# Optimization experiments

Hardware: AMD Instinct MI355X
Metric: run time of the kernel (lower is better)

The kernel has to match this reference:

```python
import jax, jax.numpy as jnp
import numpy as np

EPS = 1e-5

def _face_normals(v, vi):
    # v: [B,V,3], vi: [F,3] -> [B,F,3]
    pts = v[:, vi]                                  # [B,F,3,3]
    n = jnp.cross(pts[:, :, 1] - pts[:, :, 0], pts[:, :, 2] - pts[:, :, 0])
    norm = jnp.linalg.norm(n, axis=-1, keepdims=True)
    return n / jnp.where(norm < EPS, 1.0, norm)

def _vert_normals(v, vi):
    fn = _face_normals(v, vi)                       # [B,F,3]
    fn_rep = jnp.repeat(fn, 3, axis=1)              # [B,3F,3] (one copy per face vertex)
    vn = jnp.zeros_like(v).at[:, vi.reshape(-1)].add(fn_rep)
    norm = jnp.linalg.norm(vn, axis=-1, keepdims=True)
    return vn / jnp.where(norm < EPS, 1.0, norm)

def _values_to_uv(values, index_image, bary_image):
    # values: [B,V,C]; index_image/bary_image: [U,U,3] -> [B,C,U,U]
    mask = jnp.all(index_image != -1, axis=-1)      # [U,U]
    idx = jnp.clip(index_image, 0, values.shape[1] - 1)
    vals = values[:, idx]                           # [B,U,U,3,C]
    uv = jnp.einsum('buvkc,uvk->bcuv', vals, bary_image.astype(values.dtype))
    return uv * mask[None, None].astype(values.dtype)

def _grid_sample_bilinear(img, gx, gy):
    # img: [B,C,H,W]; gx,gy: [N] in [-1,1]; align_corners=False, zero padding
    B, C, H, W = img.shape
    ix = ((gx + 1.0) * W - 1.0) * 0.5
    iy = ((gy + 1.0) * H - 1.0) * 0.5
    x0 = jnp.floor(ix); y0 = jnp.floor(iy)
    x1 = x0 + 1.0;      y1 = y0 + 1.0
    wx1 = ix - x0; wx0 = 1.0 - wx1
    wy1 = iy - y0; wy0 = 1.0 - wy1
    def gather(xi, yi):
        valid = (xi >= 0) & (xi < W) & (yi >= 0) & (yi < H)
        xc = jnp.clip(xi, 0, W - 1).astype(jnp.int32)
        yc = jnp.clip(yi, 0, H - 1).astype(jnp.int32)
        return img[:, :, yc, xc] * valid.astype(img.dtype)  # [B,C,N]
    return (gather(x0, y0) * (wx0 * wy0) + gather(x1, y0) * (wx1 * wy0)
          + gather(x0, y1) * (wx0 * wy1) + gather(x1, y1) * (wx1 * wy1))

def _sample_uv(values_uv, uv_coords, v2uv):
    g = uv_coords * 2.0 - 1.0                       # [T,2]
    vals = _grid_sample_bilinear(values_uv, g[:, 0], g[:, 1])  # [B,C,T]
    vals = jnp.transpose(vals, (0, 2, 1))           # [B,T,C]
    return vals[:, v2uv].mean(axis=2)               # [B,V,C]

def setup_inputs() -> dict:
    key = jax.random.key(0)
    ks = jax.random.split(key, 6)
    B, V, Fc, U, T, K = 8, 100000, 200000, 1024, 110000, 2
    verts = jax.random.normal(ks[0], (B, V, 3), jnp.float32)
    vi = jax.random.randint(ks[1], (Fc, 3), 0, V, dtype=jnp.int32)
    index_image = jax.random.randint(ks[2], (U, U, 3), 0, V, dtype=jnp.int32)
    bary_image = jax.random.uniform(ks[3], (U, U, 3), jnp.float32)
    vt = jax.random.uniform(ks[4], (T, 2), jnp.float32)
    v2uv = jax.random.randint(ks[5], (V, K), 0, T, dtype=jnp.int32)
    return {"verts": verts, "bary_image": bary_image, "vt": vt,
            "vi": vi, "index_image": index_image, "v2uv": v2uv}

def reference(verts, bary_image, vt, vi, index_image, v2uv):
    vn = _vert_normals(verts, vi)                   # [B,V,3]
    uv = _values_to_uv(vn, index_image, bary_image) # [B,3,U,U]
    return _sample_uv(uv, vt, v2uv)                 # [B,V,3]
```

## Files before the change

kernel.cpp:

```cpp
#include <hip/hip_runtime.h>

#define EPS 1e-5f

constexpr int B = 8;
constexpr int V = 100000;
constexpr int F = 200000;
constexpr int U = 1024;
constexpr int T = 110000;
constexpr int ELLCAP = 32;
constexpr int TRB = (V + 255) / 256;
constexpr int ELB = (3 * F + 255) / 256;

__global__ void pre_kernel(const float* __restrict__ verts,
                           float4* __restrict__ vertsT,
                           const int* __restrict__ vi,
                           int* __restrict__ cnt,
                           int* __restrict__ ell) {
    int blk = blockIdx.x;
    if (blk < TRB) {
        int v = blk * 256 + threadIdx.x;
        if (v >= V) return;
        float4 row[8];
#pragma unroll
        for (int b = 0; b < 8; ++b) {
            const float* p = verts + (size_t)b * V * 3 + (size_t)v * 3;
            row[b] = make_float4(p[0], p[1], p[2], 0.0f);
        }
        float4* dst = vertsT + (size_t)v * 8;
#pragma unroll
        for (int b = 0; b < 8; ++b) dst[b] = row[b];
    } else {
        int e = (blk - TRB) * 256 + threadIdx.x;
        if (e >= 3 * F) return;
        int v = vi[e];
        int pos = atomicAdd(&cnt[v], 1);
        if (pos < ELLCAP) ell[v * ELLCAP + pos] = e / 3;
    }
}

__global__ void face_normals(const float4* __restrict__ vertsT,
                             const int* __restrict__ vi,
                             float4* __restrict__ fn) {
    int id = blockIdx.x * blockDim.x + threadIdx.x;
    if (id >= F * 8) return;
    int f = id >> 3;
    int b = id & 7;

    int i0 = vi[f * 3 + 0];
    int i1 = vi[f * 3 + 1];
    int i2 = vi[f * 3 + 2];

    float4 p0 = vertsT[(size_t)i0 * 8 + b];
    float4 p1 = vertsT[(size_t)i1 * 8 + b];
    float4 p2 = vertsT[(size_t)i2 * 8 + b];

    float e1x = p1.x - p0.x, e1y = p1.y - p0.y, e1z = p1.z - p0.z;
    float e2x = p2.x - p0.x, e2y = p2.y - p0.y, e2z = p2.z - p0.z;

    float nx = e1y * e2z - e1z * e2y;
    float ny = e1z * e2x - e1x * e2z;
    float nz = e1x * e2y - e1y * e2x;

    float norm = sqrtf(nx * nx + ny * ny + nz * nz);
    float inv = (norm < EPS) ? 1.0f : (1.0f / norm);
    fn[id] = make_float4(nx * inv, ny * inv, nz * inv, 0.0f);
}

__global__ void gather_vn(const float4* __restrict__ fn,
                          const int* __restrict__ cnt,
                          const int* __restrict__ ell,
                          float4* __restrict__ vn) {
    int id = blockIdx.x * blockDim.x + threadIdx.x;
    if (id >= V * 8) return;
    int v = id >> 3;
    int b = id & 7;

    int deg = min(cnt[v], ELLCAP);
    const int* row = ell + (size_t)v * ELLCAP;

    float ax = 0.0f, ay = 0.0f, az = 0.0f;
    for (int j = 0; j < deg; ++j) {
        int f = row[j];
        float4 n = fn[(size_t)f * 8 + b];
        ax += n.x; ay += n.y; az += n.z;
    }

    float n = sqrtf(ax * ax + ay * ay + az * az);
    float inv = (n < EPS) ? 1.0f : (1.0f / n);
    vn[id] = make_float4(ax * inv, ay * inv, az * inv, 0.0f);
}

__global__ void sample_points(const float4* __restrict__ vn,
                              const int* __restrict__ index_image,
                              const float* __restrict__ bary_image,
                              const float* __restrict__ vt,
                              float4* __restrict__ vals) {
    int id = blockIdx.x * blockDim.x + threadIdx.x;
    if (id >= T * 8) return;
    int t = id >> 3;
    int b = id & 7;

    float gx = vt[t * 2 + 0];
    float gy = vt[t * 2 + 1];
    float ix = gx * (float)U - 0.5f;
    float iy = gy * (float)U - 0.5f;

    float x0f = floorf(ix);
    float y0f = floorf(iy);
    int x0 = (int)x0f;
    int y0 = (int)y0f;
    float wx1 = ix - x0f, wx0 = 1.0f - wx1;
    float wy1 = iy - y0f, wy0 = 1.0f - wy1;

    float ax = 0.0f, ay = 0.0f, az = 0.0f;

#pragma unroll
    for (int cy = 0; cy < 2; ++cy) {
        int y = y0 + cy;
        if (y < 0 || y >= U) continue;
        float wy = cy ? wy1 : wy0;
#pragma unroll
        for (int cx = 0; cx < 2; ++cx) {
            int x = x0 + cx;
            if (x < 0 || x >= U) continue;
            float w = wy * (cx ? wx1 : wx0);

            int pix = y * U + x;
            int i0 = index_image[pix * 3 + 0];
            int i1 = index_image[pix * 3 + 1];
            int i2 = index_image[pix * 3 + 2];
            float m = (i0 != -1 && i1 != -1 && i2 != -1) ? 1.0f : 0.0f;
            i0 = min(max(i0, 0), V - 1);
            i1 = min(max(i1, 0), V - 1);
            i2 = min(max(i2, 0), V - 1);

            float b0 = bary_image[pix * 3 + 0];
            float b1 = bary_image[pix * 3 + 1];
            float b2 = bary_image[pix * 3 + 2];

            float4 q0 = vn[(size_t)i0 * 8 + b];
            float4 q1 = vn[(size_t)i1 * 8 + b];
            float4 q2 = vn[(size_t)i2 * 8 + b];

            float wm = w * m;
            float wb0 = wm * b0, wb1 = wm * b1, wb2 = wm * b2;
            ax += wb0 * q0.x + wb1 * q1.x + wb2 * q2.x;
            ay += wb0 * q0.y + wb1 * q1.y + wb2 * q2.y;
            az += wb0 * q0.z + wb1 * q1.z + wb2 * q2.z;
        }
    }

    vals[id] = make_float4(ax, ay, az, 0.0f);
}

__global__ void gather_out(const float4* __restrict__ vals,
                           const int* __restrict__ v2uv,
                           float* __restrict__ out) {
    int id = blockIdx.x * blockDim.x + threadIdx.x;
    if (id >= V * 8) return;
    int v = id >> 3;
    int b = id & 7;

    int t0 = v2uv[v * 2 + 0];
    int t1 = v2uv[v * 2 + 1];
    float4 x = vals[(size_t)t0 * 8 + b];
    float4 y = vals[(size_t)t1 * 8 + b];

    float* o = out + (size_t)b * V * 3 + (size_t)v * 3;
    o[0] = 0.5f * (x.x + y.x);
    o[1] = 0.5f * (x.y + y.y);
    o[2] = 0.5f * (x.z + y.z);
}

extern "C" void kernel_launch(void* const* d_in, const int* in_sizes, int n_in,
                              void* d_out, int out_size, void* d_ws, size_t ws_size,
                              hipStream_t stream) {
    const float* verts   = (const float*)d_in[0];
    const float* bary    = (const float*)d_in[1];
    const float* vt      = (const float*)d_in[2];
    const int*   vi      = (const int*)d_in[3];
    const int*   idx_img = (const int*)d_in[4];
    const int*   v2uv    = (const int*)d_in[5];
    float* out = (float*)d_out;

    float4* vertsT = (float4*)d_ws;
    float4* vn     = vertsT;
    float4* fn     = vertsT + (size_t)V * 8;
    float4* vals   = fn;
    int*    cnt    = (int*)(fn + (size_t)F * 8);
    int*    ell    = cnt + V;

    hipMemsetAsync(cnt, 0, (size_t)V * sizeof(int), stream);

    const int BLK = 256;
    pre_kernel<<<TRB + ELB, BLK, 0, stream>>>(verts, vertsT, vi, cnt, ell);
    face_normals<<<(F * 8 + BLK - 1) / BLK, BLK, 0, stream>>>(vertsT, vi, fn);
    gather_vn<<<(V * 8 + BLK - 1) / BLK, BLK, 0, stream>>>(fn, cnt, ell, vn);
    sample_points<<<(T * 8 + BLK - 1) / BLK, BLK, 0, stream>>>(
        vn, idx_img, bary, vt, vals);
    gather_out<<<(V * 8 + BLK - 1) / BLK, BLK, 0, stream>>>(vals, v2uv, out);
}
```

Before: 207.8 us.

## Fuse ELL build, face normals and per-texel corner precompute into one launch

The memset is replaced by zeroing the counters inside the transpose kernel. ELL construction, face-normal computation and a new per-texel corner precompute (index-image lookup, mask, bilinear and barycentric weights) are merged into one kernel. sample_points then reads the compact Corner records instead of recomputing them for each of the 8 batches. This cuts launches and removes redundant index/bary image loads, at the cost of an extra workspace buffer and writing and reading the corner array.

Measured after the change: 208.0 us. About the same (+0.1%).

```diff
diff --git a/kernel.cpp b/kernel.cpp
--- a/kernel.cpp
+++ b/kernel.cpp
@@ -8,14 +8,18 @@
 constexpr int U = 1024;
 constexpr int T = 110000;
 constexpr int ELLCAP = 32;
+
 constexpr int TRB = (V + 255) / 256;
+constexpr int CZB = (V + 255) / 256;
 constexpr int ELB = (3 * F + 255) / 256;
-
-__global__ void pre_kernel(const float* __restrict__ verts,
-                           float4* __restrict__ vertsT,
-                           const int* __restrict__ vi,
-                           int* __restrict__ cnt,
-                           int* __restrict__ ell) {
+constexpr int FNB = (F * 8 + 255) / 256;
+constexpr int CPB = (T + 255) / 256;
+
+struct Corner { int i0, i1, i2; float w0, w1, w2; };
+
+__global__ void k1_pre(const float* __restrict__ verts,
+                       float4* __restrict__ vertsT,
+                       int* __restrict__ cnt) {
     int blk = blockIdx.x;
     if (blk < TRB) {
         int v = blk * 256 + threadIdx.x;
@@ -30,40 +34,99 @@
 #pragma unroll
         for (int b = 0; b < 8; ++b) dst[b] = row[b];
     } else {
-        int e = (blk - TRB) * 256 + threadIdx.x;
+        int i = (blk - TRB) * 256 + threadIdx.x;
+        if (i < V) cnt[i] = 0;
+    }
+}
+
+__global__ void k2_fused(const int* __restrict__ vi,
+                         int* __restrict__ cnt,
+                         int* __restrict__ ell,
+                         const float4* __restrict__ vertsT,
+                         float4* __restrict__ fn,
+                         const int* __restrict__ index_image,
+                         const float* __restrict__ bary_image,
+                         const float* __restrict__ vt,
+                         Corner* __restrict__ corners) {
+    int blk = blockIdx.x;
+
+    if (blk < ELB) {
+        int e = blk * 256 + threadIdx.x;
         if (e >= 3 * F) return;
         int v = vi[e];
         int pos = atomicAdd(&cnt[v], 1);
         if (pos < ELLCAP) ell[v * ELLCAP + pos] = e / 3;
-    }
-}
-
-__global__ void face_normals(const float4* __restrict__ vertsT,
-                             const int* __restrict__ vi,
-                             float4* __restrict__ fn) {
-    int id = blockIdx.x * blockDim.x + threadIdx.x;
-    if (id >= F * 8) return;
-    int f = id >> 3;
-    int b = id & 7;
-
-    int i0 = vi[f * 3 + 0];
-    int i1 = vi[f * 3 + 1];
-    int i2 = vi[f * 3 + 2];
-
-    float4 p0 = vertsT[(size_t)i0 * 8 + b];
-    float4 p1 = vertsT[(size_t)i1 * 8 + b];
-    float4 p2 = vertsT[(size_t)i2 * 8 + b];
-
-    float e1x = p1.x - p0.x, e1y = p1.y - p0.y, e1z = p1.z - p0.z;
-    float e2x = p2.x - p0.x, e2y = p2.y - p0.y, e2z = p2.z - p0.z;
-
-    float nx = e1y * e2z - e1z * e2y;
-    float ny = e1z * e2x - e1x * e2z;
-    float nz = e1x * e2y - e1y * e2x;
-
-    float norm = sqrtf(nx * nx + ny * ny + nz * nz);
-    float inv = (norm < EPS) ? 1.0f : (1.0f / norm);
-    fn[id] = make_float4(nx * inv, ny * inv, nz * inv, 0.0f);
+        return;
+    }
+
+    if (blk < ELB + FNB) {
+        int id = (blk - ELB) * 256 + threadIdx.x;
+        if (id >= F * 8) return;
+        int f = id >> 3;
+        int b = id & 7;
+
+        int i0 = vi[f * 3 + 0];
+        int i1 = vi[f * 3 + 1];
+        int i2 = vi[f * 3 + 2];
+
+        float4 p0 = vertsT[(size_t)i0 * 8 + b];
+        float4 p1 = vertsT[(size_t)i1 * 8 + b];
+        float4 p2 = vertsT[(size_t)i2 * 8 + b];
+
+        float e1x = p1.x - p0.x, e1y = p1.y - p0.y, e1z = p1.z - p0.z;
+        float e2x = p2.x - p0.x, e2y = p2.y - p0.y, e2z = p2.z - p0.z;
+
+        float nx = e1y * e2z - e1z * e2y;
+        float ny = e1z * e2x - e1x * e2z;
+        float nz = e1x * e2y - e1y * e2x;
+
+        float norm = sqrtf(nx * nx + ny * ny + nz * nz);
+        float inv = (norm < EPS) ? 1.0f : (1.0f / norm);
+        fn[id] = make_float4(nx * inv, ny * inv, nz * inv, 0.0f);
+        return;
+    }
+
+    int t = (blk - ELB - FNB) * 256 + threadIdx.x;
+    if (t >= T) return;
+
+    float gx = vt[t * 2 + 0];
+    float gy = vt[t * 2 + 1];
+    float ix = gx * (float)U - 0.5f;
+    float iy = gy * (float)U - 0.5f;
+
+    float x0f = floorf(ix);
+    float y0f = floorf(iy);
+    int x0 = (int)x0f;
+    int y0 = (int)y0f;
+    float wx1 = ix - x0f, wx0 = 1.0f - wx1;
+    float wy1 = iy - y0f, wy0 = 1.0f - wy1;
+
+#pragma unroll
+    for (int c = 0; c < 4; ++c) {
+        int cy = c >> 1, cx = c & 1;
+        int y = y0 + cy;
+        int x = x0 + cx;
+        Corner cr;
+        if (x >= 0 && x < U && y >= 0 && y < U) {
+            float w = (cy ? wy1 : wy0) * (cx ? wx1 : wx0);
+            int pix = y * U + x;
+            int i0 = index_image[pix * 3 + 0];
+            int i1 = index_image[pix * 3 + 1];
+            int i2 = index_image[pix * 3 + 2];
+            float m = (i0 != -1 && i1 != -1 && i2 != -1) ? 1.0f : 0.0f;
+            float wm = w * m;
+            cr.i0 = min(max(i0, 0), V - 1);
+            cr.i1 = min(max(i1, 0), V - 1);
+            cr.i2 = min(max(i2, 0), V - 1);
+            cr.w0 = wm * bary_image[pix * 3 + 0];
+            cr.w1 = wm * bary_image[pix * 3 + 1];
+            cr.w2 = wm * bary_image[pix * 3 + 2];
+        } else {
+            cr.i0 = 0; cr.i1 = 0; cr.i2 = 0;
+            cr.w0 = 0.0f; cr.w1 = 0.0f; cr.w2 = 0.0f;
+        }
+        corners[t * 4 + c] = cr;
+    }
 }
 
 __global__ void gather_vn(const float4* __restrict__ fn,
@@ -91,63 +154,23 @@
 }
 
 __global__ void sample_points(const float4* __restrict__ vn,
-                              const int* __restrict__ index_image,
-                              const float* __restrict__ bary_image,
-                              const float* __restrict__ vt,
+                              const Corner* __restrict__ corners,
                               float4* __restrict__ vals) {
     int id = blockIdx.x * blockDim.x + threadIdx.x;
     if (id >= T * 8) return;
     int t = id >> 3;
     int b = id & 7;
 
-    float gx = vt[t * 2 + 0];
-    float gy = vt[t * 2 + 1];
-    float ix = gx * (float)U - 0.5f;
-    float iy = gy * (float)U - 0.5f;
-
-    float x0f = floorf(ix);
-    float y0f = floorf(iy);
-    int x0 = (int)x0f;
-    int y0 = (int)y0f;
-    float wx1 = ix - x0f, wx0 = 1.0f - wx1;
-    float wy1 = iy - y0f, wy0 = 1.0f - wy1;
-
     float ax = 0.0f, ay = 0.0f, az = 0.0f;
-
-#pragma unroll
-    for (int cy = 0; cy < 2; ++cy) {
-        int y = y0 + cy;
-        if (y < 0 || y >= U) continue;
-        float wy = cy ? wy1 : wy0;
-#pragma unroll
-        for (int cx = 0; cx < 2; ++cx) {
-            int x = x0 + cx;
-            if (x < 0 || x >= U) continue;
-            float w = wy * (cx ? wx1 : wx0);
-
-            int pix = y * U + x;
-            int i0 = index_image[pix * 3 + 0];
-            int i1 = index_image[pix * 3 + 1];
-            int i2 = index_image[pix * 3 + 2];
-            float m = (i0 != -1 && i1 != -1 && i2 != -1) ? 1.0f : 0.0f;
-            i0 = min(max(i0, 0), V - 1);
-            i1 = min(max(i1, 0), V - 1);
-            i2 = min(max(i2, 0), V - 1);
-
-            float b0 = bary_image[pix * 3 + 0];
-            float b1 = bary_image[pix * 3 + 1];
-            float b2 = bary_image[pix * 3 + 2];
-
-            float4 q0 = vn[(size_t)i0 * 8 + b];
-            float4 q1 = vn[(size_t)i1 * 8 + b];
-            float4 q2 = vn[(size_t)i2 * 8 + b];
-
-            float wm = w * m;
-            float wb0 = wm * b0, wb1 = wm * b1, wb2 = wm * b2;
-            ax += wb0 * q0.x + wb1 * q1.x + wb2 * q2.x;
-            ay += wb0 * q0.y + wb1 * q1.y + wb2 * q2.y;
-            az += wb0 * q0.z + wb1 * q1.z + wb2 * q2.z;
-        }
+#pragma unroll
+    for (int c = 0; c < 4; ++c) {
+        Corner cr = corners[t * 4 + c];
+        float4 q0 = vn[(size_t)cr.i0 * 8 + b];
+        float4 q1 = vn[(size_t)cr.i1 * 8 + b];
+        float4 q2 = vn[(size_t)cr.i2 * 8 + b];
+        ax += cr.w0 * q0.x + cr.w1 * q1.x + cr.w2 * q2.x;
+        ay += cr.w0 * q0.y + cr.w1 * q1.y + cr.w2 * q2.y;
+        az += cr.w0 * q0.z + cr.w1 * q1.z + cr.w2 * q2.z;
     }
 
     vals[id] = make_float4(ax, ay, az, 0.0f);
@@ -183,20 +206,19 @@
     const int*   v2uv    = (const int*)d_in[5];
     float* out = (float*)d_out;
 
-    float4* vertsT = (float4*)d_ws;
-    float4* vn     = vertsT;
-    float4* fn     = vertsT + (size_t)V * 8;
-    float4* vals   = fn;
-    int*    cnt    = (int*)(fn + (size_t)F * 8);
-    int*    ell    = cnt + V;
-
-    hipMemsetAsync(cnt, 0, (size_t)V * sizeof(int), stream);
+    float4* vertsT  = (float4*)d_ws;
+    float4* vn      = vertsT;
+    float4* fn      = vertsT + (size_t)V * 8;
+    float4* vals    = fn;
+    int*    cnt     = (int*)(fn + (size_t)F * 8);
+    int*    ell     = cnt + V;
+    Corner* corners = (Corner*)(ell + (size_t)V * ELLCAP);
 
     const int BLK = 256;
-    pre_kernel<<<TRB + ELB, BLK, 0, stream>>>(verts, vertsT, vi, cnt, ell);
-    face_normals<<<(F * 8 + BLK - 1) / BLK, BLK, 0, stream>>>(vertsT, vi, fn);
+    k1_pre<<<TRB + CZB, BLK, 0, stream>>>(verts, vertsT, cnt);
+    k2_fused<<<ELB + FNB + CPB, BLK, 0, stream>>>(
+        vi, cnt, ell, vertsT, fn, idx_img, bary, vt, corners);
     gather_vn<<<(V * 8 + BLK - 1) / BLK, BLK, 0, stream>>>(fn, cnt, ell, vn);
-    sample_points<<<(T * 8 + BLK - 1) / BLK, BLK, 0, stream>>>(
-        vn, idx_img, bary, vt, vals);
+    sample_points<<<(T * 8 + BLK - 1) / BLK, BLK, 0, stream>>>(vn, corners, vals);
     gather_out<<<(V * 8 + BLK - 1) / BLK, BLK, 0, stream>>>(vals, v2uv, out);
 }
```
